# Performance work log

Hardware: AMD Instinct MI355X
Metric: run time of the kernel (lower is better)

The kernel has to match this reference:

```python
import jax, jax.numpy as jnp
import numpy as np

R, C = 9, 9  # local window (rows, cols)


def setup_inputs() -> dict:
    key = jax.random.key(0)
    k1, k2, k3, k4, k5 = jax.random.split(key, 5)
    q = jax.random.normal(k1, (8, 256, 128, 128), jnp.float32)      # (B, q_size, H, W)
    c_t = jax.random.normal(k2, (8, 256, 512), jnp.float32)          # (B, T, c_size)
    W_a = jax.random.normal(k3, (512, 256), jnp.float32) * 0.04      # Linear(q_size -> c_size), no bias
    W_p = jax.random.normal(k4, (256, 512), jnp.float32) * 0.04      # Linear(c_size -> p_size)
    V_p = jax.random.normal(k5, (2, 256), jnp.float32) * 0.06        # Linear(p_size -> 2)
    return {"q": q, "c_t": c_t, "W_a": W_a, "W_p": W_p, "V_p": V_p}


def reference(q, c_t, W_a, W_p, V_p):
    B, D, H, W = q.shape
    T = c_t.shape[1]
    S = H  # q.size(2) before padding

    # predictive alignment: p_t = S * sigmoid(V_p(tanh(W_p(c_t))))  -> (B, T, 2)
    p_t = S * jax.nn.sigmoid(jnp.tanh(c_t @ W_p.T) @ V_p.T)

    # pad top/left with NaN, flatten spatial dims
    qp = jnp.pad(q, ((0, 0), (0, 0), (1, 0), (1, 0)), constant_values=jnp.nan)
    rows, cols = H + 1, W + 1
    qf = qp.reshape(B, D, rows * cols).transpose(0, 2, 1)  # (B, rows*cols, D)

    roff = jnp.arange(-(R // 2), (R + 1) // 2)  # R offsets
    coff = jnp.arange(-(C // 2), (C + 1) // 2)  # C offsets
    r = jnp.clip(jnp.round(p_t[..., 0]).astype(jnp.int32)[..., None] + roff + 1, 0, rows) % rows  # (B,T,R)
    c = jnp.clip(jnp.round(p_t[..., 1]).astype(jnp.int32)[..., None] + coff + 1, 0, cols) % cols  # (B,T,C)

    # flat window indices, order i*C + j (matches torch stack order)
    s = (r[..., :, None] * cols + c[..., None, :]).reshape(B, T, R * C)

    # gather windows: (B, T, R*C, D)
    qg = jnp.take_along_axis(qf, s.reshape(B, T * R * C, 1), axis=1).reshape(B, T, R * C, D)
    nan_loc = jnp.isnan(qg[..., 0])                    # (B, T, R*C)
    qg = jnp.where(nan_loc[..., None], 0.0, qg)

    # Gaussian positional weighting
    rexp = -2.0 * ((jnp.clip(r - 1, 0, None).astype(jnp.float32) - p_t[..., 0:1]) / (R // 2)) ** 2
    cexp = -2.0 * ((jnp.clip(c - 1, 0, None).astype(jnp.float32) - p_t[..., 1:2]) / (C // 2)) ** 2
    gauss = jnp.exp((rexp[..., :, None] + cexp[..., None, :]).reshape(B, T, R * C))

    # score: (W_a q) . c_t  -> (B, T, R*C)
    a_t = jnp.einsum('btkd,cd,btc->btk', qg, W_a, c_t)
    a_t = jnp.where(nan_loc, -jnp.inf, a_t)
    W_attn = jax.nn.softmax(a_t, axis=2) * gauss

    out = jnp.einsum('btk,btkd->btd', W_attn, qg)  # (B, T, D)
    return out
```

## Files before the change

### kernel.cpp

```cpp
#include <hip/hip_runtime.h>
#include <hip/hip_bf16.h>
#include <math.h>

#define Bq 8
#define Tt 256
#define Dd 256
#define Hh 128
#define Ww 128
#define Cc 512
#define HW (Hh*Ww)
#define NBT (Bq*Tt)

__global__ __launch_bounds__(256) void transpose_wp(
    const float* __restrict__ W_p, float* __restrict__ WpT)
{
    __shared__ float tile[32][33];
    const int bx = blockIdx.x;
    const int by = blockIdx.y;
    const int lx = threadIdx.x & 31, ly = threadIdx.x >> 5;
#pragma unroll
    for (int j = 0; j < 4; j++) {
        int p = by * 32 + ly + j * 8;
        tile[ly + j * 8][lx] = W_p[(size_t)p * Cc + bx * 32 + lx];
    }
    __syncthreads();
#pragma unroll
    for (int j = 0; j < 4; j++) {
        int c = bx * 32 + ly + j * 8;
        WpT[(size_t)c * 256 + by * 32 + lx] = tile[lx][ly + j * 8];
    }
}

#define TOK 8
__global__ __launch_bounds__(512) void prep_kernel(
    const float* __restrict__ c_t,
    const float* __restrict__ W_a,
    const float* __restrict__ WpT,
    const float* __restrict__ V_p,
    float* __restrict__ u_ws,
    float* __restrict__ p_ws)
{
    __shared__ float y0s[TOK][256];
    __shared__ float y1s[TOK][256];
    const int tid  = threadIdx.x;
    const int o    = tid & 255;
    const int half = tid >> 8;
    const int bt0  = blockIdx.x * TOK;

    const float* Wcol = (half ? WpT : W_a) + o;
    const float* ct0  = c_t + (size_t)bt0 * Cc;

    float acc[TOK];
#pragma unroll
    for (int t = 0; t < TOK; t++) acc[t] = 0.f;

    for (int c = 0; c < Cc; c += 4) {
        float w0 = Wcol[(size_t)(c + 0) * 256];
        float w1 = Wcol[(size_t)(c + 1) * 256];
        float w2 = Wcol[(size_t)(c + 2) * 256];
        float w3 = Wcol[(size_t)(c + 3) * 256];
#pragma unroll
        for (int t = 0; t < TOK; t++) {
            const float* r = ct0 + t * Cc + c;
            float c0 = r[0], c1 = r[1], c2 = r[2], c3 = r[3];
            acc[t] = fmaf(c0, w0, acc[t]);
            acc[t] = fmaf(c1, w1, acc[t]);
            acc[t] = fmaf(c2, w2, acc[t]);
            acc[t] = fmaf(c3, w3, acc[t]);
        }
    }

    if (half == 0) {
#pragma unroll
        for (int t = 0; t < TOK; t++)
            u_ws[(size_t)(bt0 + t) * Dd + o] = acc[t];
    } else {
        float v0 = V_p[o], v1 = V_p[256 + o];
#pragma unroll
        for (int t = 0; t < TOK; t++) {
            float th = tanhf(acc[t]);
            y0s[t][o] = th * v0;
            y1s[t][o] = th * v1;
        }
    }
    __syncthreads();

    const int wv = tid >> 6, ln = tid & 63;
    float s0 = y0s[wv][ln] + y0s[wv][ln + 64] + y0s[wv][ln + 128] + y0s[wv][ln + 192];
    float s1 = y1s[wv][ln] + y1s[wv][ln + 64] + y1s[wv][ln + 128] + y1s[wv][ln + 192];
#pragma unroll
    for (int of = 32; of >= 1; of >>= 1) {
        s0 += __shfl_xor(s0, of);
        s1 += __shfl_xor(s1, of);
    }
    if (ln == 0) {
        p_ws[(size_t)(bt0 + wv) * 2 + 0] = 128.f / (1.f + expf(-s0));
        p_ws[(size_t)(bt0 + wv) * 2 + 1] = 128.f / (1.f + expf(-s1));
    }
}

__global__ __launch_bounds__(256) void attn_kernel(
    const float* __restrict__ q,
    const float* __restrict__ u_ws,
    const float* __restrict__ p_ws,
    float* __restrict__ out)
{
    __shared__ __hip_bfloat16 win[81][258];
    __shared__ float u_s[Dd];
    __shared__ float a_red[243];
    __shared__ int   off_s[81];
    __shared__ float w_s[81];
    __shared__ float a_s[81];
    __shared__ float e_s[81];
    __shared__ float rex_s[9], cex_s[9];
    __shared__ int   rr_s[9], cc_s[9];
    __shared__ float m_sh, inv_sh;

    const int tid = threadIdx.x;
    int bt = blockIdx.x;
    bt = ((bt & 7) << 8) | (bt >> 3);
    const int b = bt >> 8;

    u_s[tid] = u_ws[(size_t)bt * Dd + tid];

    if (tid < 18) {
        int   i = (tid < 9) ? tid : tid - 9;
        float p = p_ws[(size_t)bt * 2 + ((tid < 9) ? 0 : 1)];
        int base = (int)rintf(p);
        int v = base + i - 3;
        v = min(max(v, 0), 129) % 129;
        float cl = (float)max(v - 1, 0);
        float z  = (cl - p) * 0.25f;
        float ex = -2.f * z * z;
        if (tid < 9) { rr_s[i] = v; rex_s[i] = ex; }
        else         { cc_s[i] = v; cex_s[i] = ex; }
    }
    __syncthreads();

    if (tid < 81) {
        int i = (tid * 57) >> 9;
        int j = tid - i * 9;
        int r = rr_s[i], c = cc_s[j];
        bool valid = (r > 0) && (c > 0);
        off_s[tid] = valid ? ((r - 1) * Ww + (c - 1)) : -1;
    }
    __syncthreads();

    if (tid < 243) {
        const int k = tid % 81;
        const int s = tid / 81;
        const int o = max(off_s[k], 0);
        const float* qp = q + ((size_t)(b * Dd + s)) * HW + o;
        const size_t st = (size_t)3 * HW;
        float ap = 0.f;
        int d = s;
        if (s == 0) {
            float x = qp[0];
            win[k][0] = __float2bfloat16(x);
            ap = fmaf(x, u_s[0], ap);
            qp += st; d = 3;
        }
        for (int it = 0; it < 17; it++) {
            float x0 = qp[0];
            float x1 = qp[st];
            float x2 = qp[2 * st];
            float x3 = qp[3 * st];
            float x4 = qp[4 * st];
            win[k][d     ] = __float2bfloat16(x0);
            win[k][d + 3 ] = __float2bfloat16(x1);
            win[k][d + 6 ] = __float2bfloat16(x2);
            win[k][d + 9 ] = __float2bfloat16(x3);
            win[k][d + 12] = __float2bfloat16(x4);
            ap = fmaf(x0, u_s[d     ], ap);
            ap = fmaf(x1, u_s[d + 3 ], ap);
            ap = fmaf(x2, u_s[d + 6 ], ap);
            ap = fmaf(x3, u_s[d + 9 ], ap);
            ap = fmaf(x4, u_s[d + 12], ap);
            qp += 5 * st;
            d  += 15;
        }
        a_red[tid] = ap;
    }
    __syncthreads();

    float a_val = -INFINITY;
    bool  valid_k = false;
    if (tid < 81) {
        valid_k = (off_s[tid] >= 0);
        float a = a_red[tid] + a_red[tid + 81] + a_red[tid + 162];
        a_val = valid_k ? a : -INFINITY;
        a_s[tid] = a_val;
    }
    __syncthreads();

    if (tid < 64) {
        float m = a_s[tid];
        if (tid + 64 < 81) m = fmaxf(m, a_s[tid + 64]);
        for (int o = 32; o >= 1; o >>= 1) m = fmaxf(m, __shfl_xor(m, o));
        if (tid == 0) m_sh = m;
    }
    __syncthreads();
    {
        float e = 0.f;
        if (tid < 81 && valid_k) e = expf(a_val - m_sh);
        if (tid < 81) e_s[tid] = e;
    }
    __syncthreads();
    if (tid < 64) {
        float sv = e_s[tid] + ((tid + 64 < 81) ? e_s[tid + 64] : 0.f);
        for (int o = 32; o >= 1; o >>= 1) sv += __shfl_xor(sv, o);
        if (tid == 0) inv_sh = 1.f / sv;
    }
    __syncthreads();
    if (tid < 81) {
        int i = (tid * 57) >> 9;
        int j = tid - i * 9;
        float g = expf(rex_s[i] + cex_s[j]);
        w_s[tid] = e_s[tid] * inv_sh * g;
    }
    __syncthreads();

    float acc = 0.f;
#pragma unroll
    for (int k = 0; k < 81; k++)
        acc = fmaf(w_s[k], __bfloat162float(win[k][tid]), acc);
    out[(size_t)bt * Dd + tid] = acc;
}

extern "C" void kernel_launch(void* const* d_in, const int* in_sizes, int n_in,
                              void* d_out, int out_size, void* d_ws, size_t ws_size,
                              hipStream_t stream) {
    const float* q   = (const float*)d_in[0];
    const float* c_t = (const float*)d_in[1];
    const float* W_a = (const float*)d_in[2];
    const float* W_p = (const float*)d_in[3];
    const float* V_p = (const float*)d_in[4];
    float* out  = (float*)d_out;
    float* u_ws = (float*)d_ws;
    float* p_ws = u_ws + (size_t)NBT * Dd;
    float* WpT  = p_ws + (size_t)NBT * 2;

    transpose_wp<<<dim3(16, 8), 256, 0, stream>>>(W_p, WpT);
    prep_kernel<<<NBT / TOK, 512, 0, stream>>>(c_t, W_a, WpT, V_p, u_ws, p_ws);
    attn_kernel<<<NBT, 256, 0, stream>>>(q, u_ws, p_ws, out);
}
```

Measured before the change: 290.4 us.

## Drop LDS window cache, re-gather q in weighted sum; split prep K across 1024 threads

The attention kernel no longer stages the 81x256 gathered window in LDS as bf16. The final weighted sum instead re-reads q directly from global memory, relying on L2/cache hits from the first gather pass. This frees a large LDS allocation, which should allow more blocks per CU, and removes the bf16 rounding. The prep kernel now uses 1024 threads, splits the 512-long reduction into two halves and combines the partial sums through shared memory, doubling parallelism per block. The risk is that the second gather of q costs extra global or cache traffic.

After: 370.5 us. 27.6% more time.

```diff
diff --git a/kernel.cpp b/kernel.cpp
--- a/kernel.cpp
+++ b/kernel.cpp
@@ -1,5 +1,4 @@
 #include <hip/hip_runtime.h>
-#include <hip/hip_bf16.h>
 #include <math.h>
 
 #define Bq 8
@@ -32,7 +31,7 @@
 }
 
 #define TOK 8
-__global__ __launch_bounds__(512) void prep_kernel(
+__global__ __launch_bounds__(1024) void prep_kernel(
     const float* __restrict__ c_t,
     const float* __restrict__ W_a,
     const float* __restrict__ WpT,
@@ -40,63 +39,70 @@
     float* __restrict__ u_ws,
     float* __restrict__ p_ws)
 {
+    __shared__ float part[TOK][512];
     __shared__ float y0s[TOK][256];
     __shared__ float y1s[TOK][256];
-    const int tid  = threadIdx.x;
-    const int o    = tid & 255;
-    const int half = tid >> 8;
-    const int bt0  = blockIdx.x * TOK;
-
-    const float* Wcol = (half ? WpT : W_a) + o;
-    const float* ct0  = c_t + (size_t)bt0 * Cc;
+    const int tid   = threadIdx.x;
+    const int col   = tid & 511;
+    const int chalf = tid >> 9;
+    const int bt0   = blockIdx.x * TOK;
+
+    const int  colIn = col & 255;
+    const float* Wm  = (col < 256) ? W_a : WpT;
+    const float* Wcol = Wm + colIn;
+    const float* ct0  = c_t + (size_t)bt0 * Cc + chalf * 256;
+    const int c0 = chalf * 256;
 
     float acc[TOK];
 #pragma unroll
     for (int t = 0; t < TOK; t++) acc[t] = 0.f;
 
-    for (int c = 0; c < Cc; c += 4) {
-        float w0 = Wcol[(size_t)(c + 0) * 256];
-        float w1 = Wcol[(size_t)(c + 1) * 256];
-        float w2 = Wcol[(size_t)(c + 2) * 256];
-        float w3 = Wcol[(size_t)(c + 3) * 256];
+    for (int c = 0; c < 256; c += 4) {
+        float w0 = Wcol[(size_t)(c0 + c + 0) * 256];
+        float w1 = Wcol[(size_t)(c0 + c + 1) * 256];
+        float w2 = Wcol[(size_t)(c0 + c + 2) * 256];
+        float w3 = Wcol[(size_t)(c0 + c + 3) * 256];
 #pragma unroll
         for (int t = 0; t < TOK; t++) {
             const float* r = ct0 + t * Cc + c;
-            float c0 = r[0], c1 = r[1], c2 = r[2], c3 = r[3];
-            acc[t] = fmaf(c0, w0, acc[t]);
-            acc[t] = fmaf(c1, w1, acc[t]);
-            acc[t] = fmaf(c2, w2, acc[t]);
-            acc[t] = fmaf(c3, w3, acc[t]);
-        }
-    }
-
-    if (half == 0) {
-#pragma unroll
-        for (int t = 0; t < TOK; t++)
-            u_ws[(size_t)(bt0 + t) * Dd + o] = acc[t];
-    } else {
-        float v0 = V_p[o], v1 = V_p[256 + o];
-#pragma unroll
-        for (int t = 0; t < TOK; t++) {
-            float th = tanhf(acc[t]);
-            y0s[t][o] = th * v0;
-            y1s[t][o] = th * v1;
+            acc[t] = fmaf(r[0], w0, acc[t]);
+            acc[t] = fmaf(r[1], w1, acc[t]);
+            acc[t] = fmaf(r[2], w2, acc[t]);
+            acc[t] = fmaf(r[3], w3, acc[t]);
+        }
+    }
+
+    if (chalf == 1) {
+#pragma unroll
+        for (int t = 0; t < TOK; t++) part[t][col] = acc[t];
+    }
+    __syncthreads();
+
+    if (chalf == 0) {
+        if (col < 256) {
+#pragma unroll
+            for (int t = 0; t < TOK; t++)
+                u_ws[(size_t)(bt0 + t) * Dd + col] = acc[t] + part[t][col];
+        } else {
+            float v0 = V_p[colIn], v1 = V_p[256 + colIn];
+#pragma unroll
+            for (int t = 0; t < TOK; t++) {
+                float th = tanhf(acc[t] + part[t][col]);
+                y0s[t][colIn] = th * v0;
+                y1s[t][colIn] = th * v1;
+            }
         }
     }
     __syncthreads();
 
     const int wv = tid >> 6, ln = tid & 63;
-    float s0 = y0s[wv][ln] + y0s[wv][ln + 64] + y0s[wv][ln + 128] + y0s[wv][ln + 192];
-    float s1 = y1s[wv][ln] + y1s[wv][ln + 64] + y1s[wv][ln + 128] + y1s[wv][ln + 192];
-#pragma unroll
-    for (int of = 32; of >= 1; of >>= 1) {
-        s0 += __shfl_xor(s0, of);
-        s1 += __shfl_xor(s1, of);
-    }
-    if (ln == 0) {
-        p_ws[(size_t)(bt0 + wv) * 2 + 0] = 128.f / (1.f + expf(-s0));
-        p_ws[(size_t)(bt0 + wv) * 2 + 1] = 128.f / (1.f + expf(-s1));
-    }
+    const int t  = wv & 7;
+    const float* ys = (wv < 8) ? &y0s[t][0] : &y1s[t][0];
+    float s = ys[ln] + ys[ln + 64] + ys[ln + 128] + ys[ln + 192];
+#pragma unroll
+    for (int of = 32; of >= 1; of >>= 1) s += __shfl_xor(s, of);
+    if (ln == 0)
+        p_ws[(size_t)(bt0 + t) * 2 + ((wv < 8) ? 0 : 1)] = 128.f / (1.f + expf(-s));
 }
 
 __global__ __launch_bounds__(256) void attn_kernel(
@@ -105,7 +111,6 @@
     const float* __restrict__ p_ws,
     float* __restrict__ out)
 {
-    __shared__ __hip_bfloat16 win[81][258];
     __shared__ float u_s[Dd];
     __shared__ float a_red[243];
     __shared__ int   off_s[81];
@@ -155,9 +160,7 @@
         float ap = 0.f;
         int d = s;
         if (s == 0) {
-            float x = qp[0];
-            win[k][0] = __float2bfloat16(x);
-            ap = fmaf(x, u_s[0], ap);
+            ap = fmaf(qp[0], u_s[0], ap);
             qp += st; d = 3;
         }
         for (int it = 0; it < 17; it++) {
@@ -166,11 +169,6 @@
             float x2 = qp[2 * st];
             float x3 = qp[3 * st];
             float x4 = qp[4 * st];
-            win[k][d     ] = __float2bfloat16(x0);
-            win[k][d + 3 ] = __float2bfloat16(x1);
-            win[k][d + 6 ] = __float2bfloat16(x2);
-            win[k][d + 9 ] = __float2bfloat16(x3);
-            win[k][d + 12] = __float2bfloat16(x4);
             ap = fmaf(x0, u_s[d     ], ap);
             ap = fmaf(x1, u_s[d + 3 ], ap);
             ap = fmaf(x2, u_s[d + 6 ], ap);
@@ -220,10 +218,28 @@
     }
     __syncthreads();
 
+    const float* qb = q + ((size_t)(b * Dd + tid)) * HW;
     float acc = 0.f;
-#pragma unroll
-    for (int k = 0; k < 81; k++)
-        acc = fmaf(w_s[k], __bfloat162float(win[k][tid]), acc);
+    for (int kk = 0; kk < 81; kk += 9) {
+        float x0 = qb[max(off_s[kk    ], 0)];
+        float x1 = qb[max(off_s[kk + 1], 0)];
+        float x2 = qb[max(off_s[kk + 2], 0)];
+        float x3 = qb[max(off_s[kk + 3], 0)];
+        float x4 = qb[max(off_s[kk + 4], 0)];
+        float x5 = qb[max(off_s[kk + 5], 0)];
+        float x6 = qb[max(off_s[kk + 6], 0)];
+        float x7 = qb[max(off_s[kk + 7], 0)];
+        float x8 = qb[max(off_s[kk + 8], 0)];
+        acc = fmaf(w_s[kk    ], x0, acc);
+        acc = fmaf(w_s[kk + 1], x1, acc);
+        acc = fmaf(w_s[kk + 2], x2, acc);
+        acc = fmaf(w_s[kk + 3], x3, acc);
+        acc = fmaf(w_s[kk + 4], x4, acc);
+        acc = fmaf(w_s[kk + 5], x5, acc);
+        acc = fmaf(w_s[kk + 6], x6, acc);
+        acc = fmaf(w_s[kk + 7], x7, acc);
+        acc = fmaf(w_s[kk + 8], x8, acc);
+    }
     out[(size_t)bt * Dd + tid] = acc;
 }
 
@@ -241,6 +257,6 @@
     float* WpT  = p_ws + (size_t)NBT * 2;
 
     transpose_wp<<<dim3(16, 8), 256, 0, stream>>>(W_p, WpT);
-    prep_kernel<<<NBT / TOK, 512, 0, stream>>>(c_t, W_a, WpT, V_p, u_ws, p_ws);
+    prep_kernel<<<NBT / TOK, 1024, 0, stream>>>(c_t, W_a, WpT, V_p, u_ws, p_ws);
     attn_kernel<<<NBT, 256, 0, stream>>>(q, u_ws, p_ws, out);
 }
```

## Load attention window rows with float4 reads into fp16 shared tile

Applied to the files above, without the earlier changes.

The attention kernel now stages each of the 9 window rows as three aligned 4-float segments (12 columns) per channel, using float4 global loads, instead of 81 scalar gathers per channel. Values go into a [D][9][12] fp16 shared tile and are indexed by column offset in both the score and weighted-sum loops. This cuts the number of global load instructions and gives more coalesced access, at the cost of reading a few extra columns, an extra tile zeroing pass, and fp16 instead of bf16 storage. The prep GEMV loop is also unrolled from 4 to 8 columns per step.

Result: faster. 267.8 us (-7.8%).

```diff
diff --git a/kernel.cpp b/kernel.cpp
--- a/kernel.cpp
+++ b/kernel.cpp
@@ -1,5 +1,4 @@
 #include <hip/hip_runtime.h>
-#include <hip/hip_bf16.h>
 #include <math.h>
 
 #define Bq 8
@@ -54,19 +53,26 @@
 #pragma unroll
     for (int t = 0; t < TOK; t++) acc[t] = 0.f;
 
-    for (int c = 0; c < Cc; c += 4) {
+    for (int c = 0; c < Cc; c += 8) {
         float w0 = Wcol[(size_t)(c + 0) * 256];
         float w1 = Wcol[(size_t)(c + 1) * 256];
         float w2 = Wcol[(size_t)(c + 2) * 256];
         float w3 = Wcol[(size_t)(c + 3) * 256];
+        float w4 = Wcol[(size_t)(c + 4) * 256];
+        float w5 = Wcol[(size_t)(c + 5) * 256];
+        float w6 = Wcol[(size_t)(c + 6) * 256];
+        float w7 = Wcol[(size_t)(c + 7) * 256];
 #pragma unroll
         for (int t = 0; t < TOK; t++) {
             const float* r = ct0 + t * Cc + c;
-            float c0 = r[0], c1 = r[1], c2 = r[2], c3 = r[3];
-            acc[t] = fmaf(c0, w0, acc[t]);
-            acc[t] = fmaf(c1, w1, acc[t]);
-            acc[t] = fmaf(c2, w2, acc[t]);
-            acc[t] = fmaf(c3, w3, acc[t]);
+            acc[t] = fmaf(r[0], w0, acc[t]);
+            acc[t] = fmaf(r[1], w1, acc[t]);
+            acc[t] = fmaf(r[2], w2, acc[t]);
+            acc[t] = fmaf(r[3], w3, acc[t]);
+            acc[t] = fmaf(r[4], w4, acc[t]);
+            acc[t] = fmaf(r[5], w5, acc[t]);
+            acc[t] = fmaf(r[6], w6, acc[t]);
+            acc[t] = fmaf(r[7], w7, acc[t]);
         }
     }
 
@@ -105,10 +111,9 @@
     const float* __restrict__ p_ws,
     float* __restrict__ out)
 {
-    __shared__ __hip_bfloat16 win[81][258];
+    __shared__ __align__(16) _Float16 win[Dd][9][12];
     __shared__ float u_s[Dd];
     __shared__ float a_red[243];
-    __shared__ int   off_s[81];
     __shared__ float w_s[81];
     __shared__ float a_s[81];
     __shared__ float e_s[81];
@@ -122,6 +127,13 @@
     const int b = bt >> 8;
 
     u_s[tid] = u_ws[(size_t)bt * Dd + tid];
+
+    {
+        float4* wf = (float4*)&win[0][0][0];
+        for (int i = tid; i < (int)(sizeof(win) / 16); i += 256) {
+            wf[i] = make_float4(0.f, 0.f, 0.f, 0.f);
+        }
+    }
 
     if (tid < 18) {
         int   i = (tid < 9) ? tid : tid - 9;
@@ -137,47 +149,74 @@
     }
     __syncthreads();
 
-    if (tid < 81) {
-        int i = (tid * 57) >> 9;
-        int j = tid - i * 9;
-        int r = rr_s[i], c = cc_s[j];
-        bool valid = (r > 0) && (c > 0);
-        off_s[tid] = valid ? ((r - 1) * Ww + (c - 1)) : -1;
+    int jc0 = 0, c0 = 1;
+#pragma unroll
+    for (int j = 8; j >= 0; j--)
+        if (cc_s[j] > 0) { jc0 = j; c0 = cc_s[j]; }
+    const int cb = min((c0 - 1) & ~3, Ww - 12);
+    const int e0 = (c0 - 1) - cb;
+
+    {
+        const int g  = tid >> 5;
+        const int l5 = tid & 31;
+        const bool lact = (l5 < 27);
+        const int li = lact ? ((l5 * 171) >> 9) : 0;
+        const int lv = l5 - li * 3;
+        const int vr = lact ? rr_s[li] : 0;
+        const int rowoff = (max(vr, 1) - 1) * Ww + cb + 4 * lv;
+        const float* qb = q + (size_t)b * Dd * HW;
+        if (lact && vr > 0) {
+            for (int dd = 0; dd < Dd; dd += 32) {
+                const int d0 = dd + g;
+                float4 x0 = *(const float4*)(qb + (size_t)(d0     ) * HW + rowoff);
+                float4 x1 = *(const float4*)(qb + (size_t)(d0 +  8) * HW + rowoff);
+                float4 x2 = *(const float4*)(qb + (size_t)(d0 + 16) * HW + rowoff);
+                float4 x3 = *(const float4*)(qb + (size_t)(d0 + 24) * HW + rowoff);
+                union { _Float16 h[4]; uint2 u; } p0, p1, p2, p3;
+                p0.h[0] = (_Float16)x0.x; p0.h[1] = (_Float16)x0.y;
+                p0.h[2] = (_Float16)x0.z; p0.h[3] = (_Float16)x0.w;
+                p1.h[0] = (_Float16)x1.x; p1.h[1] = (_Float16)x1.y;
+                p1.h[2] = (_Float16)x1.z; p1.h[3] = (_Float16)x1.w;
+                p2.h[0] = (_Float16)x2.x; p2.h[1] = (_Float16)x2.y;
+                p2.h[2] = (_Float16)x2.z; p2.h[3] = (_Float16)x2.w;
+                p3.h[0] = (_Float16)x3.x; p3.h[1] = (_Float16)x3.y;
+                p3.h[2] = (_Float16)x3.z; p3.h[3] = (_Float16)x3.w;
+                *(uint2*)&win[d0     ][li][4 * lv] = p0.u;
+                *(uint2*)&win[d0 +  8][li][4 * lv] = p1.u;
+                *(uint2*)&win[d0 + 16][li][4 * lv] = p2.u;
+                *(uint2*)&win[d0 + 24][li][4 * lv] = p3.u;
+            }
+        }
     }
     __syncthreads();
 
     if (tid < 243) {
-        const int k = tid % 81;
-        const int s = tid / 81;
-        const int o = max(off_s[k], 0);
-        const float* qp = q + ((size_t)(b * Dd + s)) * HW + o;
-        const size_t st = (size_t)3 * HW;
+        const int k  = tid % 81;
+        const int s  = tid / 81;
+        const int ki = (k * 57) >> 9;
+        const int kj = k - ki * 9;
+        const int pos = min(max(e0 + kj - jc0, 0), 11);
+        const _Float16* wp = &win[0][ki][pos];
         float ap = 0.f;
         int d = s;
         if (s == 0) {
-            float x = qp[0];
-            win[k][0] = __float2bfloat16(x);
-            ap = fmaf(x, u_s[0], ap);
-            qp += st; d = 3;
-        }
+            ap = fmaf((float)wp[0], u_s[0], ap);
+            d = 3;
+        }
+        const _Float16* w = wp + (size_t)d * 108;
         for (int it = 0; it < 17; it++) {
-            float x0 = qp[0];
-            float x1 = qp[st];
-            float x2 = qp[2 * st];
-            float x3 = qp[3 * st];
-            float x4 = qp[4 * st];
-            win[k][d     ] = __float2bfloat16(x0);
-            win[k][d + 3 ] = __float2bfloat16(x1);
-            win[k][d + 6 ] = __float2bfloat16(x2);
-            win[k][d + 9 ] = __float2bfloat16(x3);
-            win[k][d + 12] = __float2bfloat16(x4);
+            float x0 = (float)w[0];
+            float x1 = (float)w[3 * 108];
+            float x2 = (float)w[6 * 108];
+            float x3 = (float)w[9 * 108];
+            float x4 = (float)w[12 * 108];
             ap = fmaf(x0, u_s[d     ], ap);
             ap = fmaf(x1, u_s[d + 3 ], ap);
             ap = fmaf(x2, u_s[d + 6 ], ap);
             ap = fmaf(x3, u_s[d + 9 ], ap);
             ap = fmaf(x4, u_s[d + 12], ap);
-            qp += 5 * st;
-            d  += 15;
+            w += 15 * 108;
+            d += 15;
         }
         a_red[tid] = ap;
     }
@@ -186,7 +225,9 @@
     float a_val = -INFINITY;
     bool  valid_k = false;
     if (tid < 81) {
-        valid_k = (off_s[tid] >= 0);
+        const int ki = (tid * 57) >> 9;
+        const int kj = tid - ki * 9;
+        valid_k = (rr_s[ki] > 0) && (cc_s[kj] > 0);
         float a = a_red[tid] + a_red[tid + 81] + a_red[tid + 162];
         a_val = valid_k ? a : -INFINITY;
         a_s[tid] = a_val;
@@ -220,10 +261,16 @@
     }
     __syncthreads();
 
+    int posj[9];
+#pragma unroll
+    for (int j = 0; j < 9; j++) posj[j] = min(max(e0 + j - jc0, 0), 11);
+    const _Float16* wd = &win[tid][0][0];
     float acc = 0.f;
 #pragma unroll
-    for (int k = 0; k < 81; k++)
-        acc = fmaf(w_s[k], __bfloat162float(win[k][tid]), acc);
+    for (int k = 0; k < 81; k++) {
+        const int ki = k / 9, kj = k % 9;
+        acc = fmaf(w_s[k], (float)wd[ki * 12 + posj[kj]], acc);
+    }
     out[(size_t)bt * Dd + tid] = acc;
 }
 
```
